# Kernel tuning notes

Measured on AMD Instinct MI355X. Metric: run time of the kernel, lower is better.

The kernel has to match this reference:

```python
import jax, jax.numpy as jnp
import numpy as np

N = 100000   # nodes (single node type)
E = 160000   # edges per relation
R = 4        # relations
D_IN = 128
D_OUT = 128


def setup_inputs() -> dict:
    key = jax.random.key(0)
    k_x, k_w, k_lw, k_s, k_d = jax.random.split(key, 5)
    x = jax.random.normal(k_x, (N, D_IN), dtype=jnp.float32)
    # xavier-ish scale for weights
    scale = np.float32(np.sqrt(2.0 / (D_IN + D_OUT)))
    W = jax.random.normal(k_w, (R, D_IN, D_OUT), dtype=jnp.float32) * scale
    loop_weight = jax.random.normal(k_lw, (D_IN, D_OUT), dtype=jnp.float32) * scale
    src = jax.random.randint(k_s, (R, E), 0, N, dtype=jnp.int64)
    dst = jax.random.randint(k_d, (R, E), 0, N, dtype=jnp.int64)
    return {"x": x, "W": W, "loop_weight": loop_weight, "src": src, "dst": dst}


def reference(x, W, loop_weight, src, dst):
    # Per-relation linear transform: [R, N, D_OUT]
    h = jnp.einsum('nd,rde->rne', x, W)

    def rel_aggregate(hr, s, d):
        # gather messages at src, sum into dst, normalize by dst in-degree ('right' norm)
        msg = hr[s]                                            # [E, D_OUT]
        agg = jax.ops.segment_sum(msg, d, num_segments=N)      # [N, D_OUT]
        deg = jax.ops.segment_sum(jnp.ones(s.shape, hr.dtype), d, num_segments=N)
        return agg / jnp.clip(deg, 1.0)[:, None]

    per_rel = jax.vmap(rel_aggregate)(h, src, dst)             # [R, N, D_OUT]
    out = per_rel.sum(axis=0) + x @ loop_weight                # sum over relations + self-loop
    return jax.nn.relu(out)                                    # activation; dropout=0 -> identity
```

## Files before the change

### kernel.cpp

```cpp
#include <hip/hip_runtime.h>

#define D 128
#define TN 64
#define NC 8

typedef __attribute__((ext_vector_type(8))) short short8;
typedef __attribute__((ext_vector_type(4))) float f32x4;

__device__ __forceinline__ unsigned int bf16rne(float f) {
  unsigned int b = __float_as_uint(f);
  return (b + 0x7fffu + ((b >> 16) & 1u)) >> 16;
}
__device__ __forceinline__ float bf2f(unsigned int u) {
  return __uint_as_float(u << 16);
}

__global__ __launch_bounds__(256) void rgc_prep(
    const float* __restrict__ x, const float* __restrict__ W,
    const float* __restrict__ loopW, unsigned short* __restrict__ xb,
    unsigned short* __restrict__ WT, uint4* __restrict__ zbase,
    long long zb16, int R, long long total8, int xblocks, int wblocks)
{
  if ((int)blockIdx.x < xblocks) {
    long long i = (long long)blockIdx.x * 256 + threadIdx.x;
    if (i >= total8) return;
    float4 v0 = ((const float4*)x)[i * 2];
    float4 v1 = ((const float4*)x)[i * 2 + 1];
    uint4 u;
    u.x = bf16rne(v0.x) | (bf16rne(v0.y) << 16);
    u.y = bf16rne(v0.z) | (bf16rne(v0.w) << 16);
    u.z = bf16rne(v1.x) | (bf16rne(v1.y) << 16);
    u.w = bf16rne(v1.z) | (bf16rne(v1.w) << 16);
    ((uint4*)xb)[i] = u;
  } else if ((int)blockIdx.x < xblocks + wblocks) {
    int tid = (blockIdx.x - xblocks) * 256 + threadIdx.x;
    int s = tid >> 14;
    if (s > R) return;
    int rem = tid & 16383;
    int k = rem >> 7;
    int c = rem & 127;
    float v = (s < R) ? W[(size_t)s * D * D + k * D + c] : loopW[k * D + c];
    unsigned int u = bf16rne(v);
    unsigned int off = ((unsigned int)(c * D + k) * 2u) ^ (((unsigned int)(c & 7)) << 4);
    *(unsigned short*)((char*)WT + (size_t)s * D * D * 2 + off) = (unsigned short)u;
  } else {
    long long i = (long long)(blockIdx.x - xblocks - wblocks) * 256 + threadIdx.x;
    if (i < zb16) zbase[i] = make_uint4(0, 0, 0, 0);
  }
}

__global__ __launch_bounds__(256) void rgc_hist(
    const int* __restrict__ dst, int* __restrict__ cnt8, int N, int E, int R)
{
  int r = blockIdx.y;
  int e = blockIdx.x * 256 + threadIdx.x;
  if (e >= E) return;
  int k = (blockIdx.x + gridDim.x * blockIdx.y) & (NC - 1);
  int d = dst[(size_t)r * E + e];
  atomicAdd(&cnt8[((size_t)k * R + r) * N + d], 1);
}

__global__ __launch_bounds__(256) void rgc_offsets(
    const int* __restrict__ cnt8, int* __restrict__ rowctr8,
    int* __restrict__ off8, int2* __restrict__ npd,
    int N, int E, int R, int nt256, int nchunks)
{
  __shared__ int wtot[4];
  __shared__ int wbase[4];
  __shared__ int sbase;

  int chunk = blockIdx.x;
  if (chunk >= nchunks) return;
  int kx = blockIdx.x & (NC - 1);
  int r = chunk / nt256, t = chunk - r * nt256;
  int tid = threadIdx.x;
  int wv = tid >> 6, lane = tid & 63;
  int node = t * 256 + tid;

  int ck[NC];
  int deg = 0;
  if (node < N) {
#pragma unroll
    for (int k = 0; k < NC; k++) {
      ck[k] = cnt8[((size_t)k * R + r) * N + node];
      deg += ck[k];
    }
  } else {
#pragma unroll
    for (int k = 0; k < NC; k++) ck[k] = 0;
  }
  int v = deg;
#pragma unroll
  for (int o = 1; o < 64; o <<= 1) {
    int tsh = __shfl_up(v, o, 64);
    if (lane >= o) v += tsh;
  }
  if (lane == 63) wtot[wv] = v;
  __syncthreads();
  if (tid == 0) {
    int run = 0;
#pragma unroll
    for (int i = 0; i < 4; i++) { wbase[i] = run; run += wtot[i]; }
    sbase = atomicAdd(&rowctr8[kx * R + r], run);
  }
  __syncthreads();

  if (node < N) {
    int start = (kx * R + r) * E + sbase + wbase[wv] + (v - deg);
    npd[(size_t)r * N + node] = make_int2(start, deg);
    int run = start;
#pragma unroll
    for (int k = 0; k < NC; k++) {
      off8[((size_t)k * R + r) * N + node] = run;
      run += ck[k];
    }
  }
}

__global__ __launch_bounds__(256) void rgc_fill(
    const int* __restrict__ src, const int* __restrict__ dst,
    int* __restrict__ off8, int* __restrict__ esrc, int N, int E, int R)
{
  int r = blockIdx.y;
  int e = blockIdx.x * 256 + threadIdx.x;
  if (e >= E) return;
  int k = (blockIdx.x + gridDim.x * blockIdx.y) & (NC - 1);
  int d = dst[(size_t)r * E + e];
  int pos = atomicAdd(&off8[((size_t)k * R + r) * N + d], 1);
  esrc[pos] = src[(size_t)r * E + e];
}

__global__ __launch_bounds__(256) void rgc_agg(
    const unsigned short* __restrict__ xb, const int2* __restrict__ npd,
    const int* __restrict__ esrc, unsigned short* __restrict__ Ahat,
    int N, int R, int tile0)
{
  int tx = threadIdx.x;
  int ltile = blockIdx.x;
  int tile = tile0 + ltile;
  int r = blockIdx.y;
  int node0 = tile * TN;
  int grp = tx >> 4, c = tx & 15;
  char* dstp = (char*)(Ahat + ((size_t)ltile * R + r) * (TN * D));

#pragma unroll
  for (int t = 0; t < 4; t++) {
    int row = grp * 4 + t;
    int node = node0 + row;
    float a[8];
#pragma unroll
    for (int q = 0; q < 8; q++) a[q] = 0.f;
    int deg = 0;
    if (node < N) {
      int2 sd = npd[(size_t)r * N + node];
      int st = sd.x;
      deg = sd.y;
      int j = 0;
      for (; j + 2 <= deg; j += 2) {
        int s0 = esrc[st + j];
        int s1 = esrc[st + j + 1];
        uint4 u0 = ((const uint4*)(xb + (size_t)s0 * D))[c];
        uint4 u1 = ((const uint4*)(xb + (size_t)s1 * D))[c];
        a[0] += bf2f(u0.x & 0xffffu) + bf2f(u1.x & 0xffffu);
        a[1] += bf2f(u0.x >> 16)     + bf2f(u1.x >> 16);
        a[2] += bf2f(u0.y & 0xffffu) + bf2f(u1.y & 0xffffu);
        a[3] += bf2f(u0.y >> 16)     + bf2f(u1.y >> 16);
        a[4] += bf2f(u0.z & 0xffffu) + bf2f(u1.z & 0xffffu);
        a[5] += bf2f(u0.z >> 16)     + bf2f(u1.z >> 16);
        a[6] += bf2f(u0.w & 0xffffu) + bf2f(u1.w & 0xffffu);
        a[7] += bf2f(u0.w >> 16)     + bf2f(u1.w >> 16);
      }
      if (j < deg) {
        int s0 = esrc[st + j];
        uint4 u0 = ((const uint4*)(xb + (size_t)s0 * D))[c];
        a[0] += bf2f(u0.x & 0xffffu); a[1] += bf2f(u0.x >> 16);
        a[2] += bf2f(u0.y & 0xffffu); a[3] += bf2f(u0.y >> 16);
        a[4] += bf2f(u0.z & 0xffffu); a[5] += bf2f(u0.z >> 16);
        a[6] += bf2f(u0.w & 0xffffu); a[7] += bf2f(u0.w >> 16);
      }
    }
    float sc = 1.0f / fmaxf((float)deg, 1.0f);
    uint4 o;
    o.x = bf16rne(a[0] * sc) | (bf16rne(a[1] * sc) << 16);
    o.y = bf16rne(a[2] * sc) | (bf16rne(a[3] * sc) << 16);
    o.z = bf16rne(a[4] * sc) | (bf16rne(a[5] * sc) << 16);
    o.w = bf16rne(a[6] * sc) | (bf16rne(a[7] * sc) << 16);
    unsigned int off =
        ((unsigned int)(row * 256 + c * 16)) ^ (((unsigned int)(row & 7)) << 4);
    *(uint4*)(dstp + off) = o;
  }
}

__global__ __launch_bounds__(256) void rgc_gemm(
    const unsigned short* __restrict__ xb, const unsigned short* __restrict__ WT,
    const unsigned short* __restrict__ Ahat, float* __restrict__ out,
    int N, int R, int tile0)
{
  __shared__ char Ab[TN * D * 2];
  __shared__ char Wb[D * D * 2];

  int tx = threadIdx.x;
  int ltile = blockIdx.x;
  int tile = tile0 + ltile;
  int node0 = tile * TN;
  int lane = tx & 63;
  int w = tx >> 6;

  f32x4 acc[4][2];
#pragma unroll
  for (int i = 0; i < 4; i++)
#pragma unroll
    for (int j = 0; j < 2; j++) acc[i][j] = (f32x4){0.f, 0.f, 0.f, 0.f};

  unsigned int kof = (unsigned int)((lane >> 4) * 16);

  for (int s = 0; s <= R; s++) {
    bool is_loop = (s == R);
    if (!is_loop) {
      const float4* asrc = (const float4*)(Ahat + ((size_t)ltile * R + s) * (TN * D));
#pragma unroll
      for (int i = 0; i < 4; i++)
        ((float4*)Ab)[tx + i * 256] = asrc[tx + i * 256];
    } else {
#pragma unroll
      for (int it = 0; it < 4; it++) {
        int i = tx + it * 256;
        int row = i >> 4, c16 = i & 15;
        int node = node0 + row;
        uint4 u = make_uint4(0, 0, 0, 0);
        if (node < N) u = ((const uint4*)(xb + (size_t)node * D))[c16];
        unsigned int off =
            ((unsigned int)(row * 256 + c16 * 16)) ^ (((unsigned int)(row & 7)) << 4);
        *(uint4*)(Ab + off) = u;
      }
    }
    const float4* wsrc = (const float4*)(WT + (size_t)s * D * D);
#pragma unroll
    for (int i = 0; i < 8; i++)
      ((float4*)Wb)[tx + i * 256] = wsrc[tx + i * 256];
    __syncthreads();

    short8 bfr[2][4];
#pragma unroll
    for (int ctl = 0; ctl < 2; ctl++) {
      int rB = (2 * w + ctl) * 16 + (lane & 15);
      unsigned int mB = (unsigned int)((rB & 7) << 4);
#pragma unroll
      for (int kk = 0; kk < 4; kk++)
        bfr[ctl][kk] =
            *(const short8*)(Wb + rB * 256 + (((unsigned int)(kk * 64) + kof) ^ mB));
    }
#pragma unroll
    for (int rt = 0; rt < 4; rt++) {
      int rA = rt * 16 + (lane & 15);
      unsigned int mA = (unsigned int)((rA & 7) << 4);
      short8 afr[4];
#pragma unroll
      for (int kk = 0; kk < 4; kk++)
        afr[kk] =
            *(const short8*)(Ab + rA * 256 + (((unsigned int)(kk * 64) + kof) ^ mA));
#pragma unroll
      for (int ctl = 0; ctl < 2; ctl++)
#pragma unroll
        for (int kk = 0; kk < 4; kk++)
          acc[rt][ctl] = __builtin_amdgcn_mfma_f32_16x16x32_bf16(
              afr[kk], bfr[ctl][kk], acc[rt][ctl], 0, 0, 0);
    }
    __syncthreads();
  }

  int colb = lane & 15;
  int rowb = (lane >> 4) * 4;
#pragma unroll
  for (int rt = 0; rt < 4; rt++) {
#pragma unroll
    for (int ctl = 0; ctl < 2; ctl++) {
      int ct = 2 * w + ctl;
#pragma unroll
      for (int j = 0; j < 4; j++) {
        int node = node0 + rt * 16 + rowb + j;
        if (node < N)
          out[(size_t)node * D + ct * 16 + colb] = fmaxf(acc[rt][ctl][j], 0.f);
      }
    }
  }
}

extern "C" void kernel_launch(void* const* d_in, const int* in_sizes, int n_in,
                              void* d_out, int out_size, void* d_ws, size_t ws_size,
                              hipStream_t stream)
{
  const float* x     = (const float*)d_in[0];
  const float* W     = (const float*)d_in[1];
  const float* loopW = (const float*)d_in[2];
  const int*   src   = (const int*)d_in[3];
  const int*   dst   = (const int*)d_in[4];
  float* out = (float*)d_out;

  int N = in_sizes[0] / D;
  int R = in_sizes[1] / (D * D);
  int E = in_sizes[3] / R;
  int ntiles = (N + TN - 1) / TN;
  int ctmax = (ntiles + 1) / 2;

  size_t o_cnt8  = 0;
  size_t o_rowc  = o_cnt8 + (size_t)NC * R * N * 4;
  size_t o_off8  = (o_rowc + (size_t)NC * R * 4 + 15) & ~(size_t)15;
  size_t o_npd   = (o_off8 + (size_t)NC * R * N * 4 + 15) & ~(size_t)15;
  size_t o_esrc  = (o_npd + (size_t)R * N * 8 + 15) & ~(size_t)15;
  size_t o_wt    = (o_esrc + (size_t)NC * R * E * 4 + 15) & ~(size_t)15;
  size_t o_xb    = (o_wt + (size_t)(R + 1) * D * D * 2 + 15) & ~(size_t)15;
  size_t o_ahat  = (o_xb + (size_t)N * D * 2 + 15) & ~(size_t)15;

  char* wsb = (char*)d_ws;
  int*  cnt8    = (int*)(wsb + o_cnt8);
  int*  rowctr8 = (int*)(wsb + o_rowc);
  int*  off8    = (int*)(wsb + o_off8);
  int2* npd     = (int2*)(wsb + o_npd);
  int*  esrc    = (int*)(wsb + o_esrc);
  unsigned short* WT   = (unsigned short*)(wsb + o_wt);
  unsigned short* xb   = (unsigned short*)(wsb + o_xb);
  unsigned short* Ahat = (unsigned short*)(wsb + o_ahat);

  long long total8 = (long long)N * D / 8;
  int xblocks = (int)((total8 + 255) / 256);
  int wblocks = ((R + 1) * D * D + 255) / 256;
  long long zb16 = (long long)(o_off8 - o_cnt8) / 16;
  int zblocks = (int)((zb16 + 255) / 256);
  rgc_prep<<<xblocks + wblocks + zblocks, 256, 0, stream>>>(
      x, W, loopW, xb, WT, (uint4*)wsb, zb16, R, total8, xblocks, wblocks);

  dim3 egrid((E + 255) / 256, R);
  rgc_hist<<<egrid, 256, 0, stream>>>(dst, cnt8, N, E, R);
  int nt256 = (N + 255) / 256;
  int nchunks = R * nt256;
  rgc_offsets<<<nchunks, 256, 0, stream>>>(
      cnt8, rowctr8, off8, npd, N, E, R, nt256, nchunks);
  rgc_fill<<<egrid, 256, 0, stream>>>(src, dst, off8, esrc, N, E, R);

  for (int c = 0; c < 2; c++) {
    int tile0 = c * ctmax;
    int ct = (ntiles - tile0 < ctmax) ? (ntiles - tile0) : ctmax;
    if (ct <= 0) break;
    dim3 agrid(ct, R);
    rgc_agg<<<agrid, 256, 0, stream>>>(xb, npd, esrc, Ahat, N, R, tile0);
    rgc_gemm<<<ct, 256, 0, stream>>>(xb, WT, Ahat, out, N, R, tile0);
  }
}
```

Before: 184.8 us.

## Fuse CSR build kernels into one cooperative kernel with grid syncs

Merges the prep/zero, histogram, offset-scan and fill kernels into a single cooperative launch of 1024 blocks that uses grid-stride loops and grid.sync() between phases. This removes three kernel launches and the gaps between them. In exchange, each phase runs on a fixed grid that may be smaller than the original launches, grid barriers add their own cost, and the zeroing range is now computed from NC*R*N+NC*R instead of the workspace offsets.

```diff
diff --git a/kernel.cpp b/kernel.cpp
--- a/kernel.cpp
+++ b/kernel.cpp
@@ -1,4 +1,7 @@
 #include <hip/hip_runtime.h>
+#include <hip/hip_cooperative_groups.h>
+
+namespace cg = cooperative_groups;
 
 #define D 128
 #define TN 64
@@ -15,15 +18,22 @@
   return __uint_as_float(u << 16);
 }
 
-__global__ __launch_bounds__(256) void rgc_prep(
+__global__ __launch_bounds__(256) void rgc_build(
     const float* __restrict__ x, const float* __restrict__ W,
-    const float* __restrict__ loopW, unsigned short* __restrict__ xb,
-    unsigned short* __restrict__ WT, uint4* __restrict__ zbase,
-    long long zb16, int R, long long total8, int xblocks, int wblocks)
+    const float* __restrict__ loopW, const int* __restrict__ src,
+    const int* __restrict__ dst, unsigned short* __restrict__ xb,
+    unsigned short* __restrict__ WT, int* __restrict__ cnt8,
+    int* __restrict__ rowctr8, int* __restrict__ off8,
+    int2* __restrict__ npd, int* __restrict__ esrc,
+    int N, int E, int R, long long total8, int nt256)
 {
-  if ((int)blockIdx.x < xblocks) {
-    long long i = (long long)blockIdx.x * 256 + threadIdx.x;
-    if (i >= total8) return;
+  cg::grid_group grid = cg::this_grid();
+  int tid = threadIdx.x;
+  long long gstride = (long long)gridDim.x * 256;
+  long long gbase = (long long)blockIdx.x * 256 + tid;
+  int kx = blockIdx.x & (NC - 1);
+
+  for (long long i = gbase; i < total8; i += gstride) {
     float4 v0 = ((const float4*)x)[i * 2];
     float4 v1 = ((const float4*)x)[i * 2 + 1];
     uint4 u;
@@ -32,102 +42,91 @@
     u.z = bf16rne(v1.x) | (bf16rne(v1.y) << 16);
     u.w = bf16rne(v1.z) | (bf16rne(v1.w) << 16);
     ((uint4*)xb)[i] = u;
-  } else if ((int)blockIdx.x < xblocks + wblocks) {
-    int tid = (blockIdx.x - xblocks) * 256 + threadIdx.x;
-    int s = tid >> 14;
-    if (s > R) return;
-    int rem = tid & 16383;
+  }
+  long long wtotal = (long long)(R + 1) * D * D;
+  for (long long i = gbase; i < wtotal; i += gstride) {
+    int t = (int)i;
+    int s = t >> 14;
+    int rem = t & 16383;
     int k = rem >> 7;
     int c = rem & 127;
     float v = (s < R) ? W[(size_t)s * D * D + k * D + c] : loopW[k * D + c];
     unsigned int u = bf16rne(v);
     unsigned int off = ((unsigned int)(c * D + k) * 2u) ^ (((unsigned int)(c & 7)) << 4);
     *(unsigned short*)((char*)WT + (size_t)s * D * D * 2 + off) = (unsigned short)u;
-  } else {
-    long long i = (long long)(blockIdx.x - xblocks - wblocks) * 256 + threadIdx.x;
-    if (i < zb16) zbase[i] = make_uint4(0, 0, 0, 0);
-  }
-}
-
-__global__ __launch_bounds__(256) void rgc_hist(
-    const int* __restrict__ dst, int* __restrict__ cnt8, int N, int E, int R)
-{
-  int r = blockIdx.y;
-  int e = blockIdx.x * 256 + threadIdx.x;
-  if (e >= E) return;
-  int k = (blockIdx.x + gridDim.x * blockIdx.y) & (NC - 1);
-  int d = dst[(size_t)r * E + e];
-  atomicAdd(&cnt8[((size_t)k * R + r) * N + d], 1);
-}
-
-__global__ __launch_bounds__(256) void rgc_offsets(
-    const int* __restrict__ cnt8, int* __restrict__ rowctr8,
-    int* __restrict__ off8, int2* __restrict__ npd,
-    int N, int E, int R, int nt256, int nchunks)
-{
+  }
+  long long zn4 = ((long long)NC * R * N + NC * R) / 4;
+  uint4* zp = (uint4*)cnt8;
+  for (long long i = gbase; i < zn4; i += gstride) zp[i] = make_uint4(0, 0, 0, 0);
+
+  grid.sync();
+
+  long long etot = (long long)R * E;
+  for (long long ie = gbase; ie < etot; ie += gstride) {
+    int r = (int)(ie / E);
+    int d = dst[ie];
+    atomicAdd(&cnt8[((size_t)kx * R + r) * N + d], 1);
+  }
+
+  grid.sync();
+
   __shared__ int wtot[4];
   __shared__ int wbase[4];
   __shared__ int sbase;
-
-  int chunk = blockIdx.x;
-  if (chunk >= nchunks) return;
-  int kx = blockIdx.x & (NC - 1);
-  int r = chunk / nt256, t = chunk - r * nt256;
-  int tid = threadIdx.x;
+  int nchunks = R * nt256;
   int wv = tid >> 6, lane = tid & 63;
-  int node = t * 256 + tid;
-
-  int ck[NC];
-  int deg = 0;
-  if (node < N) {
-#pragma unroll
-    for (int k = 0; k < NC; k++) {
-      ck[k] = cnt8[((size_t)k * R + r) * N + node];
-      deg += ck[k];
-    }
-  } else {
-#pragma unroll
-    for (int k = 0; k < NC; k++) ck[k] = 0;
-  }
-  int v = deg;
-#pragma unroll
-  for (int o = 1; o < 64; o <<= 1) {
-    int tsh = __shfl_up(v, o, 64);
-    if (lane >= o) v += tsh;
-  }
-  if (lane == 63) wtot[wv] = v;
-  __syncthreads();
-  if (tid == 0) {
-    int run = 0;
-#pragma unroll
-    for (int i = 0; i < 4; i++) { wbase[i] = run; run += wtot[i]; }
-    sbase = atomicAdd(&rowctr8[kx * R + r], run);
-  }
-  __syncthreads();
-
-  if (node < N) {
-    int start = (kx * R + r) * E + sbase + wbase[wv] + (v - deg);
-    npd[(size_t)r * N + node] = make_int2(start, deg);
-    int run = start;
-#pragma unroll
-    for (int k = 0; k < NC; k++) {
-      off8[((size_t)k * R + r) * N + node] = run;
-      run += ck[k];
-    }
-  }
-}
-
-__global__ __launch_bounds__(256) void rgc_fill(
-    const int* __restrict__ src, const int* __restrict__ dst,
-    int* __restrict__ off8, int* __restrict__ esrc, int N, int E, int R)
-{
-  int r = blockIdx.y;
-  int e = blockIdx.x * 256 + threadIdx.x;
-  if (e >= E) return;
-  int k = (blockIdx.x + gridDim.x * blockIdx.y) & (NC - 1);
-  int d = dst[(size_t)r * E + e];
-  int pos = atomicAdd(&off8[((size_t)k * R + r) * N + d], 1);
-  esrc[pos] = src[(size_t)r * E + e];
+  for (int chunk = blockIdx.x; chunk < nchunks; chunk += gridDim.x) {
+    int r = chunk / nt256, t = chunk - r * nt256;
+    int node = t * 256 + tid;
+
+    int ck[NC];
+    int deg = 0;
+    if (node < N) {
+#pragma unroll
+      for (int k = 0; k < NC; k++) {
+        ck[k] = cnt8[((size_t)k * R + r) * N + node];
+        deg += ck[k];
+      }
+    } else {
+#pragma unroll
+      for (int k = 0; k < NC; k++) ck[k] = 0;
+    }
+    int v = deg;
+#pragma unroll
+    for (int o = 1; o < 64; o <<= 1) {
+      int tsh = __shfl_up(v, o, 64);
+      if (lane >= o) v += tsh;
+    }
+    if (lane == 63) wtot[wv] = v;
+    __syncthreads();
+    if (tid == 0) {
+      int run = 0;
+#pragma unroll
+      for (int i = 0; i < 4; i++) { wbase[i] = run; run += wtot[i]; }
+      sbase = atomicAdd(&rowctr8[kx * R + r], run);
+    }
+    __syncthreads();
+    if (node < N) {
+      int start = (kx * R + r) * E + sbase + wbase[wv] + (v - deg);
+      npd[(size_t)r * N + node] = make_int2(start, deg);
+      int run = start;
+#pragma unroll
+      for (int k = 0; k < NC; k++) {
+        off8[((size_t)k * R + r) * N + node] = run;
+        run += ck[k];
+      }
+    }
+    __syncthreads();
+  }
+
+  grid.sync();
+
+  for (long long ie = gbase; ie < etot; ie += gstride) {
+    int r = (int)(ie / E);
+    int d = dst[ie];
+    int pos = atomicAdd(&off8[((size_t)kx * R + r) * N + d], 1);
+    esrc[pos] = src[ie];
+  }
 }
 
 __global__ __launch_bounds__(256) void rgc_agg(
@@ -323,20 +322,15 @@
   unsigned short* Ahat = (unsigned short*)(wsb + o_ahat);
 
   long long total8 = (long long)N * D / 8;
-  int xblocks = (int)((total8 + 255) / 256);
-  int wblocks = ((R + 1) * D * D + 255) / 256;
-  long long zb16 = (long long)(o_off8 - o_cnt8) / 16;
-  int zblocks = (int)((zb16 + 255) / 256);
-  rgc_prep<<<xblocks + wblocks + zblocks, 256, 0, stream>>>(
-      x, W, loopW, xb, WT, (uint4*)wsb, zb16, R, total8, xblocks, wblocks);
-
-  dim3 egrid((E + 255) / 256, R);
-  rgc_hist<<<egrid, 256, 0, stream>>>(dst, cnt8, N, E, R);
   int nt256 = (N + 255) / 256;
-  int nchunks = R * nt256;
-  rgc_offsets<<<nchunks, 256, 0, stream>>>(
-      cnt8, rowctr8, off8, npd, N, E, R, nt256, nchunks);
-  rgc_fill<<<egrid, 256, 0, stream>>>(src, dst, off8, esrc, N, E, R);
+
+  void* args[] = {
+      (void*)&x, (void*)&W, (void*)&loopW, (void*)&src, (void*)&dst,
+      (void*)&xb, (void*)&WT, (void*)&cnt8, (void*)&rowctr8, (void*)&off8,
+      (void*)&npd, (void*)&esrc, (void*)&N, (void*)&E, (void*)&R,
+      (void*)&total8, (void*)&nt256};
+  hipLaunchCooperativeKernel((const void*)rgc_build, dim3(1024), dim3(256),
+                             args, 0, stream);
 
   for (int c = 0; c < 2; c++) {
     int tile0 = c * ctmax;
```

Result: slower. 501.4 us (+171.3%).
